# Kernel optimization log

Hardware: AMD Instinct MI355X
Metric: run time of the kernel (lower is better)

## Reference

```python
import jax, jax.numpy as jnp
import numpy as np

S, B, T = 400, 32, 32          # encoder seq len, batch, max_summary_length
V, OOV, E, H = 50000, 50, 128, 256


def _p(key, shape, scale=0.05):
    return (jax.random.normal(key, shape) * scale).astype(jnp.float32)


def lstm_step(x, h, c, Wih, Whh, bih, bhh):
    # PyTorch LSTM gate order: i, f, g, o
    g = x @ Wih.T + h @ Whh.T + bih + bhh
    i, f, gg, o = jnp.split(g, 4, axis=-1)
    c = jax.nn.sigmoid(f) * c + jax.nn.sigmoid(i) * jnp.tanh(gg)
    h = jax.nn.sigmoid(o) * jnp.tanh(c)
    return h, c


def setup_inputs() -> dict:
    key = jax.random.key(0)
    ks = jax.random.split(key, 34)
    inp = {
        # token ids >= 1 so encoder_mask = clip(inputs,0,1) is all ones and
        # packed lengths == full length (PackedRNN becomes a plain LSTM)
        "inputs": jax.random.randint(ks[0], (S, B), 1, V),
        "inputs_lengths": jnp.full((B,), S, dtype=jnp.int32),
        "outputs_tokens": jax.random.randint(ks[1], (T, B), 1, V),  # teacher-forced targets
        "texts_extended": jax.random.randint(ks[2], (S, B), 1, V + OOV),
        "oov_size": OOV,
        # learned parameters
        "embedding": _p(ks[3], (V, E)).at[0].set(0.0),  # padding_idx=0
        "enc_Wih_f": _p(ks[4], (4 * H, E)), "enc_Whh_f": _p(ks[5], (4 * H, H)),
        "enc_bih_f": _p(ks[6], (4 * H,)), "enc_bhh_f": _p(ks[7], (4 * H,)),
        "enc_Wih_b": _p(ks[8], (4 * H, E)), "enc_Whh_b": _p(ks[9], (4 * H, H)),
        "enc_bih_b": _p(ks[10], (4 * H,)), "enc_bhh_b": _p(ks[11], (4 * H,)),
        "W_feat": _p(ks[12], (2 * H, 2 * H)),  # encoder.features (no bias)
        "W_rh": _p(ks[13], (H, 2 * H)), "b_rh": _p(ks[14], (H,)),
        "W_rc": _p(ks[15], (H, 2 * H)), "b_rc": _p(ks[16], (H,)),
        "W_af": _p(ks[17], (2 * H, 2 * H)), "b_af": _p(ks[18], (2 * H,)),  # attention.features
        "w_v": _p(ks[19], (2 * H,)),  # attention_first Linear(2H,1,no bias)
        "W_ctx": _p(ks[20], (E, 2 * H + E)), "b_ctx": _p(ks[21], (E,)),  # decoder.context
        "dec_Wih": _p(ks[22], (4 * H, E)), "dec_Whh": _p(ks[23], (4 * H, H)),
        "dec_bih": _p(ks[24], (4 * H,)), "dec_bhh": _p(ks[25], (4 * H,)),
        "W_pg": _p(ks[26], (1, 4 * H + E)), "b_pg": _p(ks[27], (1,)),
        "W_o1": _p(ks[28], (H, 4 * H)), "b_o1": _p(ks[29], (H,)),
        "W_o2": _p(ks[30], (V, H)), "b_o2": _p(ks[31], (V,)),
    }
    return inp


def reference(inputs, inputs_lengths, outputs_tokens, texts_extended, oov_size,
              embedding, enc_Wih_f, enc_Whh_f, enc_bih_f, enc_bhh_f,
              enc_Wih_b, enc_Whh_b, enc_bih_b, enc_bhh_b,
              W_feat, W_rh, b_rh, W_rc, b_rc, W_af, b_af, w_v,
              W_ctx, b_ctx, dec_Wih, dec_Whh, dec_bih, dec_bhh,
              W_pg, b_pg, W_o1, b_o1, W_o2, b_o2):
    Bsz = inputs.shape[1]
    emb_in = embedding[inputs]                                # [S,B,E]
    h0 = jnp.zeros((Bsz, H), jnp.float32)

    # --- bidirectional encoder LSTM (lengths == S, so packing is a no-op) ---
    def enc_f(carry, x):
        h, c = carry
        h, c = lstm_step(x, h, c, enc_Wih_f, enc_Whh_f, enc_bih_f, enc_bhh_f)
        return (h, c), h

    def enc_b(carry, x):
        h, c = carry
        h, c = lstm_step(x, h, c, enc_Wih_b, enc_Whh_b, enc_bih_b, enc_bhh_b)
        return (h, c), h

    (hf, cf), out_f = jax.lax.scan(enc_f, (h0, h0), emb_in)
    (hb, cb), out_b = jax.lax.scan(enc_b, (h0, h0), emb_in[::-1])
    out_b = out_b[::-1]
    enc_out = jnp.concatenate([out_f, out_b], -1)             # [S,B,2H]
    enc_feat = enc_out @ W_feat.T                             # [S,B,2H]
    dh0 = jax.nn.relu(jnp.concatenate([hf, hb], -1) @ W_rh.T + b_rh)  # [B,H]
    dc0 = jax.nn.relu(jnp.concatenate([cf, cb], -1) @ W_rc.T + b_rc)  # [B,H]

    mask = jnp.clip(inputs, 0, 1).astype(jnp.float32)          # [S,B]
    ctx0 = jnp.zeros((Bsz, 2 * H), jnp.float32)
    rows = jnp.arange(Bsz)[:, None]
    tex_T = texts_extended.T                                   # [B,S]

    # --- decoder loop (teacher forcing, coverage disabled: default) ---
    def dec_step(carry, tok):
        h, c, ctx = carry
        x = jnp.concatenate([ctx, embedding[tok]], 1) @ W_ctx.T + b_ctx     # [B,E]
        h, c = lstm_step(x, h, c, dec_Wih, dec_Whh, dec_bih, dec_bhh)
        dh = jnp.concatenate([h, c], 1)                                      # [B,2H]
        e = jnp.tanh(enc_feat + (dh @ W_af.T + b_af)[None]) @ w_v            # [S,B]
        a = jax.nn.softmax(e, axis=0) * mask
        a = a / a.sum(0, keepdims=True)                                      # layers.Normalize(0)
        context = jnp.einsum('sb,sbd->bd', a, enc_out)                       # [B,2H]
        p_gen = jax.nn.sigmoid(jnp.concatenate([context, dh, x], 1) @ W_pg.T + b_pg)  # [B,1]
        hid = jnp.concatenate([dh, context], 1) @ W_o1.T + b_o1              # [B,H]
        out_v = jax.nn.softmax(hid @ W_o2.T + b_o2, axis=1)                  # [B,V]
        vd = jnp.pad(p_gen * out_v, ((0, 0), (0, oov_size)))                 # [B,V+OOV]
        final = vd.at[rows, tex_T].add((1.0 - p_gen) * a.T)                  # scatter_add copy dist
        return (h, c, context), (final, a)

    _, (outs, atts) = jax.lax.scan(dec_step, (dh0, dc0, ctx0), outputs_tokens)
    return outs, atts  # [T,B,V+OOV], [T,S,B]
```

## Files before the change

kernel.cpp:

```cpp
#include <hip/hip_runtime.h>

#define DEV static __device__ __forceinline__

typedef short  s16x8 __attribute__((ext_vector_type(8)));
typedef float  f32x4 __attribute__((ext_vector_type(4)));
typedef _Float16 h2f __attribute__((ext_vector_type(2)));

constexpr int S = 400, B = 32, T = 32, V = 50000, OOV = 50, E = 128, H = 256;
constexpr int VO = V + OOV, SB = S * B;
constexpr int VP = 50048;

DEV ushort f2bf(float x) {
    union { float f; unsigned u; } a; a.f = x;
    unsigned r = (a.u + 0x7fffu + ((a.u >> 16) & 1u)) >> 16;
    return (ushort)r;
}
DEV float bf2f(unsigned b) {
    union { unsigned u; float f; } a; a.u = b << 16; return a.f;
}
DEV float sigmoidf_(float x) { return 1.0f / (1.0f + __expf(-x)); }
DEV float tanhf_(float x) { float e = __expf(2.0f * x); return 1.0f - 2.0f / (e + 1.0f); }
DEV h2f asH2(unsigned u) { union { unsigned u; h2f h; } x; x.u = u; return x.h; }

#if __has_builtin(__builtin_amdgcn_fdot2)
DEV float dot2(h2f a, h2f b, float c) { return __builtin_amdgcn_fdot2(a, b, c, false); }
#else
DEV float dot2(h2f a, h2f b, float c) { return c + (float)a.x * (float)b.x + (float)a.y * (float)b.y; }
#endif

DEV unsigned f2e4(float v) {
    union { float f; unsigned u; } a; a.f = v;
    unsigned u = a.u + 0x0007FFFFu + ((a.u >> 20) & 1u);
    int e = (int)((u >> 23) & 255) - 127 + 7;
    unsigned m = (u >> 20) & 7u;
    if (e <= 0) return 0u;
    if (e > 15) { e = 15; m = 6; }
    return (unsigned)((e << 3) | m);
}
DEV float e42f(unsigned b) {
    int e = (int)((b >> 3) & 15), m = (int)(b & 7);
    if (e == 0) return (float)m * 1.953125e-3f;
    union { unsigned u; float f; } a;
    a.u = ((unsigned)(e + 120) << 23) | ((unsigned)m << 20);
    return a.f;
}

constexpr size_t SZ_EMB2D  = (size_t)SB * E * 2;
constexpr size_t SZ_WIHCAT = (size_t)2048 * 128 * 2;
constexpr size_t SZ_BIASX  = 2048 * 4;
constexpr size_t SZ_WFEAT  = (size_t)512 * 512 * 2;
constexpr size_t SZ_WO2    = (size_t)V * H * 2;
constexpr size_t SZ_WHH2   = (size_t)2 * 64 * 512 * 16;
constexpr size_t SZ_WCAT   = (size_t)1024 * 896 * 4;
constexpr size_t SZ_BC     = 1024 * 4;
constexpr size_t SZ_CPG    = 256;
constexpr size_t SZ_WRHT   = (size_t)512 * 256 * 4;
constexpr size_t SZ_WRCT   = (size_t)512 * 256 * 4;
constexpr size_t SZ_EMBDEC = (size_t)T * B * E * 4;
constexpr size_t SZ_WZ     = 1664 * 4 + 256;
constexpr size_t SZ_WAFBF  = (size_t)512 * 512 * 2;
constexpr size_t SZ_WO1BF  = (size_t)256 * 1024 * 2;
constexpr size_t SZ_CTXACC = (size_t)(T + 2) * 16384 * 4;
constexpr size_t SZ_SSUM   = (size_t)(T + 2) * 32 * 4 + 256;
constexpr size_t SZ_XALL   = (size_t)T * B * 1024 * 2;
constexpr size_t SZ_EXPS   = (size_t)T * SB * 4;
constexpr size_t SZ_XPROJ  = (size_t)SB * 2048 * 2;
constexpr size_t SZ_ENCOUT = (size_t)SB * 512 * 2;
constexpr size_t SZ_ENCFEAT= (size_t)SB * 512 * 2;
constexpr size_t SZ_HFIN   = (size_t)2 * B * H * 4;
constexpr size_t SZ_HPP    = (size_t)2 * B * H * 4;
constexpr size_t SZ_PGEN   = (size_t)T * B * 4;
constexpr size_t SZ_HIDALL = (size_t)T * B * 256 * 2;

constexpr size_t OFF_EMB2D  = 0;
constexpr size_t OFF_WIHCAT = OFF_EMB2D  + SZ_EMB2D;
constexpr size_t OFF_BIASX  = OFF_WIHCAT + SZ_WIHCAT;
constexpr size_t OFF_WFEAT  = OFF_BIASX  + SZ_BIASX;
constexpr size_t OFF_WO2    = OFF_WFEAT  + SZ_WFEAT;
constexpr size_t OFF_WHH2   = OFF_WO2    + SZ_WO2;
constexpr size_t OFF_WCAT   = OFF_WHH2   + SZ_WHH2;
constexpr size_t OFF_BC     = OFF_WCAT   + SZ_WCAT;
constexpr size_t OFF_CPG    = OFF_BC     + SZ_BC;
constexpr size_t OFF_WRHT   = OFF_CPG    + SZ_CPG;
constexpr size_t OFF_WRCT   = OFF_WRHT   + SZ_WRHT;
constexpr size_t OFF_EMBDEC = OFF_WRCT   + SZ_WRCT;
constexpr size_t OFF_WZ     = OFF_EMBDEC + SZ_EMBDEC;
constexpr size_t OFF_WAFBF  = OFF_WZ     + SZ_WZ;
constexpr size_t OFF_WO1BF  = OFF_WAFBF  + SZ_WAFBF;
constexpr size_t OFF_CTXACC = OFF_WO1BF  + SZ_WO1BF;
constexpr size_t OFF_SSUM   = OFF_CTXACC + SZ_CTXACC;
constexpr size_t OFF_XALL   = OFF_SSUM   + SZ_SSUM;
constexpr size_t OFF_EXPS   = OFF_XALL   + SZ_XALL;
constexpr size_t OFF_XPROJ  = OFF_EXPS   + SZ_EXPS;
constexpr size_t OFF_ENCOUT = OFF_XPROJ  + SZ_XPROJ;
constexpr size_t OFF_ENCFEAT= OFF_ENCOUT + SZ_ENCOUT;
constexpr size_t OFF_HFIN   = OFF_ENCFEAT+ SZ_ENCFEAT;
constexpr size_t OFF_CFIN   = OFF_HFIN   + SZ_HFIN;
constexpr size_t OFF_HPP    = OFF_CFIN   + SZ_HFIN;
constexpr size_t OFF_CPP    = OFF_HPP    + SZ_HPP;
constexpr size_t OFF_PGEN   = OFF_CPP    + SZ_HPP;
constexpr size_t OFF_HIDALL = OFF_PGEN   + SZ_PGEN;
constexpr size_t OFF_PBUF   = OFF_XPROJ;

constexpr long P1 = 2048L*128;
constexpr long P2 = 2048;
constexpr long P3 = 512L*512;
constexpr long P4 = (long)V*H;
constexpr long P5 = 2L*64*512*4;
constexpr long P6 = 1024L*896;
constexpr long P7 = 1;
constexpr long P8 = 1024;
constexpr long P9 = (long)SB*E;
constexpr long P10 = 512L*256;
constexpr long P11 = 512L*256;
constexpr long P12 = 32L*32*128;
constexpr long P13 = 1664;
constexpr long P14 = 512L*512;
constexpr long P15 = 256L*1024;
constexpr long P16 = (long)(T+2)*16384;
constexpr long P17 = (long)(T+2)*32;
constexpr long PREP_TOTAL = P1+P2+P3+P4+P5+P6+P7+P8+P9+P10+P11+P12+P13+P14+P15+P16+P17;

__global__ __launch_bounds__(256)
void prep_kernel(const float* __restrict__ Wih_f, const float* __restrict__ Wih_b,
                 const float* __restrict__ bih_f, const float* __restrict__ bhh_f,
                 const float* __restrict__ bih_b, const float* __restrict__ bhh_b,
                 const float* __restrict__ W_feat, const float* __restrict__ W_o2,
                 const float* __restrict__ Whh_f, const float* __restrict__ Whh_b,
                 const float* __restrict__ dWih, const float* __restrict__ W_ctx,
                 const float* __restrict__ W_pg, const float* __restrict__ b_pg,
                 const float* __restrict__ b_ctx, const float* __restrict__ dbih,
                 const float* __restrict__ dbhh, const float* __restrict__ emb,
                 const int* __restrict__ inputs, const float* __restrict__ dWhh,
                 const float* __restrict__ W_rh, const float* __restrict__ W_rc,
                 const int* __restrict__ toks, const float* __restrict__ W_af,
                 const float* __restrict__ W_o1,
                 ushort* __restrict__ emb2d, ushort* __restrict__ wihcat,
                 float* __restrict__ biasx, ushort* __restrict__ wfeatbf,
                 ushort* __restrict__ wo2bf, unsigned* __restrict__ whh2,
                 float* __restrict__ wcat, float* __restrict__ cpgp,
                 float* __restrict__ bcv, float* __restrict__ wrhT,
                 float* __restrict__ wrcT, float* __restrict__ embdec,
                 float* __restrict__ wz, ushort* __restrict__ wafbf,
                 ushort* __restrict__ wo1bf, float* __restrict__ ctxAcc,
                 float* __restrict__ ssumAll)
{
    long id = (long)blockIdx.x * 256 + threadIdx.x;
    if (id < P1) { int r = id >> 7, e = id & 127;
        float v = (r < 1024) ? Wih_f[r*128+e] : Wih_b[(r-1024)*128+e];
        wihcat[id] = f2bf(v); return; }
    id -= P1;
    if (id < P2) { biasx[id] = (id < 1024) ? bih_f[id]+bhh_f[id] : bih_b[id-1024]+bhh_b[id-1024]; return; }
    id -= P2;
    if (id < P3) { wfeatbf[id] = f2bf(W_feat[id]); return; }
    id -= P3;
    if (id < P4) { wo2bf[id] = f2bf(W_o2[id]); return; }
    id -= P4;
    if (id < P5) {
        int q = id & 3; long r = id >> 2;
        int t = (int)(r & 511); r >>= 9; int c = (int)(r & 63); int dir = (int)(r >> 6);
        int gate = c >> 4, p = c & 15, kh = t & 1;
        int j = t >> 1;
        int k0 = kh * 128 + p * 8 + 2 * q;
        int row = gate * 256 + j;
        const float* W = dir ? Whh_b : Whh_f;
        h2f hv; hv.x = (_Float16)W[(size_t)row*256 + k0]; hv.y = (_Float16)W[(size_t)row*256 + k0 + 1];
        whh2[id] = __builtin_bit_cast(unsigned, hv); return; }
    id -= P5;
    if (id < P6) { int col = (int)(id / 896), k = (int)(id % 896);
        if (k < 640) {
            float acc = 0.f;
            for (int e = 0; e < 128; ++e) acc += dWih[col*128+e] * W_ctx[e*640+k];
            wcat[id] = acc;
        } else wcat[id] = dWhh[(size_t)col*256 + (k - 640)];
        return; }
    id -= P6;
    if (id < P7) { float acc = b_pg[0];
        for (int e = 0; e < 128; ++e) acc += W_pg[1024+e] * b_ctx[e];
        cpgp[0] = acc; return; }
    id -= P7;
    if (id < P8) { float acc = dbih[id] + dbhh[id];
        for (int e = 0; e < 128; ++e) acc += dWih[id*128+e] * b_ctx[e];
        bcv[id] = acc; return; }
    id -= P8;
    if (id < P9) { long sb = id >> 7; int e = id & 127;
        emb2d[id] = f2bf(emb[(size_t)inputs[sb]*128 + e]); return; }
    id -= P9;
    if (id < P10) { int j = id & 255; long k = id >> 8;
        wrhT[id] = W_rh[(size_t)j * 512 + k]; return; }
    id -= P10;
    if (id < P11) { int j = id & 255; long k = id >> 8;
        wrcT[id] = W_rc[(size_t)j * 512 + k]; return; }
    id -= P11;
    if (id < P12) { long tb = id >> 7; int e = id & 127;
        embdec[id] = emb[(size_t)toks[tb]*128 + e]; return; }
    id -= P12;
    if (id < P13) {
        int k = (int)id;
        if (k < 1024) wz[k] = W_pg[k];
        else { int u = k - 1024; float acc = 0.f;
            for (int e = 0; e < 128; ++e) acc += W_pg[1024+e] * W_ctx[e*640+u];
            wz[k] = acc; }
        return; }
    id -= P13;
    if (id < P14) { int d = id & 511; long k = id >> 9;
        wafbf[id] = f2bf(W_af[(size_t)d * 512 + k]); return; }
    id -= P14;
    if (id < P15) { wo1bf[id] = f2bf(W_o1[id]); return; }
    id -= P15;
    if (id < P16) { ctxAcc[id] = 0.f; return; }
    id -= P16;
    if (id < P17) { ssumAll[id] = (id < 64) ? 1.0f : 0.f; return; }
}

template<int BM, int BN, int NT, int MODE, bool BIAS, bool SWZ>
__global__ __launch_bounds__(NT)
void gemm_nt(const ushort* __restrict__ A, int lda, const ushort* __restrict__ Bm, int ldb,
             void* __restrict__ Cp, int ldc, const float* __restrict__ bias,
             int M, int N, int K)
{
    constexpr int WN = BN / 32;
    __shared__ ushort sA[BM * 32];
    __shared__ ushort sB[BN * 32];
    int tid = threadIdx.x, lane = tid & 63, wid = tid >> 6;
    int wm = wid / WN, wn = wid % WN;
    int mb = blockIdx.y, nb = blockIdx.x;
    if (SWZ) {
        int n = gridDim.x, x = nb & 7, y = nb >> 3, q = n >> 3, r = n & 7;
        nb = (x < r ? x * (q + 1) : r * (q + 1) + (x - r) * q) + y;
    }
    int l15 = lane & 15, lg = lane >> 4;
    f32x4 acc[2][2] = {};
    for (int k0 = 0; k0 < K; k0 += 32) {
        for (int idx = tid; idx < BM * 4; idx += NT) {
            int r = idx >> 2, kc = (idx & 3) << 3;
            int row = mb * BM + r;
            uint4 v = make_uint4(0u, 0u, 0u, 0u);
            if (row < M) v = *(const uint4*)(A + (size_t)row * lda + k0 + kc);
            *(uint4*)(&sA[r * 32 + kc]) = v;
        }
        for (int idx = tid; idx < BN * 4; idx += NT) {
            int r = idx >> 2, kc = (idx & 3) << 3;
            int row = nb * BN + r;
            uint4 v = make_uint4(0u, 0u, 0u, 0u);
            if (row < N) v = *(const uint4*)(Bm + (size_t)row * ldb + k0 + kc);
            *(uint4*)(&sB[r * 32 + kc]) = v;
        }
        __syncthreads();
        s16x8 a0 = *(const s16x8*)(&sA[(wm * 32 + l15) * 32 + lg * 8]);
        s16x8 a1 = *(const s16x8*)(&sA[(wm * 32 + 16 + l15) * 32 + lg * 8]);
        s16x8 b0 = *(const s16x8*)(&sB[(wn * 32 + l15) * 32 + lg * 8]);
        s16x8 b1 = *(const s16x8*)(&sB[(wn * 32 + 16 + l15) * 32 + lg * 8]);
        acc[0][0] = __builtin_amdgcn_mfma_f32_16x16x32_bf16(a0, b0, acc[0][0], 0, 0, 0);
        acc[0][1] = __builtin_amdgcn_mfma_f32_16x16x32_bf16(a0, b1, acc[0][1], 0, 0, 0);
        acc[1][0] = __builtin_amdgcn_mfma_f32_16x16x32_bf16(a1, b0, acc[1][0], 0, 0, 0);
        acc[1][1] = __builtin_amdgcn_mfma_f32_16x16x32_bf16(a1, b1, acc[1][1], 0, 0, 0);
        __syncthreads();
    }
    int cb = nb * BN + wn * 32, rb = mb * BM + wm * 32;
    #pragma unroll
    for (int mf = 0; mf < 2; ++mf)
    #pragma unroll
    for (int nf = 0; nf < 2; ++nf) {
        int col = cb + nf * 16 + l15;
        float bv = 0.f;
        if (BIAS) { if (col < N) bv = bias[col]; }
        #pragma unroll
        for (int r = 0; r < 4; ++r) {
            int row = rb + mf * 16 + lg * 4 + r;
            if (row < M && col < N) {
                float v = acc[mf][nf][r] + bv;
                if (MODE == 0)      ((float*)Cp)[(size_t)row * ldc + col] = v;
                else if (MODE == 1) ((ushort*)Cp)[(size_t)row * ldc + col] = __builtin_bit_cast(ushort, (_Float16)v);
                else if (MODE == 2) ((float*)Cp)[(size_t)row * ldc + col] = __expf(v);
                else if (MODE == 3) ((ushort*)Cp)[(size_t)row * ldc + col] = f2bf(v);
                else                ((unsigned char*)Cp)[(size_t)row * ldc + col] = (unsigned char)f2e4(__expf(v));
            }
        }
    }
}

__global__ __launch_bounds__(512, 2)
void enc_kernel(const ushort* __restrict__ xproj, const uint4* __restrict__ whh2,
                ushort* __restrict__ encoutB, float* __restrict__ hfin, float* __restrict__ cfin)
{
    __shared__ uint4  wlds[18 * 512];
    __shared__ __attribute__((aligned(16))) ushort hh16[2][2][136];
    int b = blockIdx.x & 31, dir = blockIdx.x >> 5;
    int t = threadIdx.x, j = t >> 1, kh = t & 1;
    const uint4* gw = whh2 + (size_t)dir * 64 * 512 + t;
    uint4 wreg[46];
    #pragma unroll
    for (int c = 0; c < 46; ++c) wreg[c] = gw[(size_t)c * 512];
    #pragma unroll
    for (int c = 46; c < 64; ++c) wlds[(c - 46) * 512 + t] = gw[(size_t)c * 512];
    if (t < 256) { hh16[0][t >> 7][t & 127] = 0; }
    float cst = 0.f, hst = 0.f;
    __syncthreads();
    const int khoff = kh * 512;
    #pragma unroll 1
    for (int step = 0; step < S; ++step) {
        int s = dir ? (S - 1 - step) : step;
        int cur = step & 1, nxt = cur ^ 1;
        const ushort* xp = xproj + ((size_t)(s * B + b)) * 2048 + dir * 1024 + j + khoff;
        ushort xra = xp[0], xrb = xp[256];
        float a0 = 0.f, a1 = 0.f, a2 = 0.f, a3 = 0.f;
        #pragma unroll
        for (int p = 0; p < 16; ++p) {
            uint4 hp = *(const uint4*)(&hh16[cur][kh][p * 8]);
            uint4 wi = wreg[p];
            uint4 wf = wreg[16 + p];
            uint4 wg = (p < 14) ? wreg[32 + p] : wlds[(p - 14) * 512 + t];
            uint4 wo = wlds[(p + 2) * 512 + t];
            h2f p0 = asH2(hp.x), p1 = asH2(hp.y), p2 = asH2(hp.z), p3 = asH2(hp.w);
            a0 = dot2(p0, asH2(wi.x), a0); a0 = dot2(p1, asH2(wi.y), a0);
            a0 = dot2(p2, asH2(wi.z), a0); a0 = dot2(p3, asH2(wi.w), a0);
            a1 = dot2(p0, asH2(wf.x), a1); a1 = dot2(p1, asH2(wf.y), a1);
            a1 = dot2(p2, asH2(wf.z), a1); a1 = dot2(p3, asH2(wf.w), a1);
            a2 = dot2(p0, asH2(wg.x), a2); a2 = dot2(p1, asH2(wg.y), a2);
            a2 = dot2(p2, asH2(wg.z), a2); a2 = dot2(p3, asH2(wg.w), a2);
            a3 = dot2(p0, asH2(wo.x), a3); a3 = dot2(p1, asH2(wo.y), a3);
            a3 = dot2(p2, asH2(wo.z), a3); a3 = dot2(p3, asH2(wo.w), a3);
        }
        float xv0 = (float)__builtin_bit_cast(_Float16, xra);
        float xv1 = (float)__builtin_bit_cast(_Float16, xrb);
        a0 += kh ? 0.f : xv0;  a1 += kh ? 0.f : xv1;
        a2 += kh ? xv0 : 0.f;  a3 += kh ? xv1 : 0.f;
        a0 += __shfl_xor(a0, 1); a1 += __shfl_xor(a1, 1);
        a2 += __shfl_xor(a2, 1); a3 += __shfl_xor(a3, 1);
        cst = sigmoidf_(a1) * cst + sigmoidf_(a0) * tanhf_(a2);
        hst = sigmoidf_(a3) * tanhf_(cst);
        if (kh == 0) {
            encoutB[((size_t)(b * S + s)) * 512 + dir * 256 + j] = f2bf(hst);
            hh16[nxt][j >> 7][j & 127] = __builtin_bit_cast(ushort, (_Float16)hst);
        }
        __syncthreads();
    }
    if (kh == 0) {
        hfin[(dir * 32 + b) * 256 + j] = hst;
        cfin[(dir * 32 + b) * 256 + j] = cst;
    }
}

__global__ __launch_bounds__(256)
void initdec_kernel(const float* __restrict__ hfin, const float* __restrict__ cfin,
                    const float* __restrict__ wrhT, const float* __restrict__ b_rh,
                    const float* __restrict__ wrcT, const float* __restrict__ b_rc,
                    float* __restrict__ hPP, float* __restrict__ cPP)
{
    int b = blockIdx.x, j = threadIdx.x;
    float ah = b_rh[j], ac = b_rc[j];
    for (int k = 0; k < 512; ++k) {
        float hv = (k < 256) ? hfin[b * 256 + k] : hfin[(32 + b) * 256 + k - 256];
        float cv = (k < 256) ? cfin[b * 256 + k] : cfin[(32 + b) * 256 + k - 256];
        ah += hv * wrhT[k * 256 + j];
        ac += cv * wrcT[k * 256 + j];
    }
    hPP[b * 256 + j] = fmaxf(ah, 0.f);
    cPP[b * 256 + j] = fmaxf(ac, 0.f);
}

__global__ __launch_bounds__(256)
void dec_lstm2_kernel(const float* __restrict__ wcat, const float* __restrict__ bcv,
                      const float* __restrict__ ctxPrevAcc, const float* __restrict__ ssumPrev,
                      const float* __restrict__ hin, const float* __restrict__ cin,
                      float* __restrict__ hout, float* __restrict__ cout,
                      const float* __restrict__ embt, ushort* __restrict__ xAll_t)
{
    __shared__ float pre[256];
    int blk = blockIdx.x, tid = threadIdx.x;
    int b = tid & 31, ci = tid >> 5;
    int gi = ci >> 1, jj = ci & 1;
    int j = (blk << 1) + jj;
    int col = gi * 256 + j;
    float rinvb = 1.0f / ssumPrev[b];
    float acc = bcv[col], accC = 0.f;
    const float4* w = (const float4*)(wcat + (size_t)col * 896);
    const float4* x0 = (const float4*)(ctxPrevAcc + b * 512);
    #pragma unroll 8
    for (int u = 0; u < 128; ++u) { float4 a = w[u], q = x0[u]; accC += a.x*q.x + a.y*q.y + a.z*q.z + a.w*q.w; }
    const float4* x1 = (const float4*)(embt + b * 128);
    #pragma unroll 8
    for (int u = 0; u < 32; ++u) { float4 a = w[128 + u], q = x1[u]; acc += a.x*q.x + a.y*q.y + a.z*q.z + a.w*q.w; }
    const float4* x2 = (const float4*)(hin + b * 256);
    #pragma unroll 8
    for (int u = 0; u < 64; ++u) { float4 a = w[160 + u], q = x2[u]; acc += a.x*q.x + a.y*q.y + a.z*q.z + a.w*q.w; }
    pre[tid] = acc + rinvb * accC;
    __syncthreads();
    if (tid < 64) {
        int b2 = tid & 31, qq = tid >> 5;
        int j2 = (blk << 1) + qq;
        float iv = pre[(0 + qq) * 32 + b2];
        float fv = pre[(2 + qq) * 32 + b2];
        float gv = pre[(4 + qq) * 32 + b2];
        float ov = pre[(6 + qq) * 32 + b2];
        float cp = cin[b2 * 256 + j2];
        float cn = sigmoidf_(fv) * cp + sigmoidf_(iv) * tanhf_(gv);
        float hn = sigmoidf_(ov) * tanhf_(cn);
        cout[b2 * 256 + j2] = cn;
        hout[b2 * 256 + j2] = hn;
        xAll_t[(size_t)b2 * 1024 + j2] = f2bf(hn);
        xAll_t[(size_t)b2 * 1024 + 256 + j2] = f2bf(cn);
    }
}

__global__ __launch_bounds__(512)
void dec_attn2_kernel(const float* __restrict__ h, const float* __restrict__ c,
                      const ushort* __restrict__ wafbf, const float* __restrict__ b_af,
                      const ushort* __restrict__ encfeatB, const float* __restrict__ wv,
                      const int* __restrict__ inputs, const ushort* __restrict__ encoutB,
                      float* __restrict__ expsT, float* __restrict__ ssumT,
                      float* __restrict__ ctxAccT)
{
    __shared__ float hc[512];
    __shared__ float dafL[512];
    __shared__ float scL[50];
    __shared__ float part8[8][512];
    int blk = blockIdx.x, tid = threadIdx.x;
    int b = blk >> 3, sc = blk & 7, s0 = sc * 50;
    int sl = tid >> 6, dth = tid & 63;
    hc[tid] = (tid < 256) ? h[b * 256 + tid] : c[b * 256 + tid - 256];
    __syncthreads();
    {
        float acc8[8] = {};
        const ushort* wbase = wafbf + (size_t)(sl * 64) * 512 + dth * 8;
        #pragma unroll 8
        for (int kk = 0; kk < 64; ++kk) {
            uint4 u = *(const uint4*)(wbase + (size_t)kk * 512);
            float hk = hc[sl * 64 + kk];
            acc8[0] += hk * bf2f(u.x & 0xffffu);
            acc8[1] += hk * bf2f(u.x >> 16);
            acc8[2] += hk * bf2f(u.y & 0xffffu);
            acc8[3] += hk * bf2f(u.y >> 16);
            acc8[4] += hk * bf2f(u.z & 0xffffu);
            acc8[5] += hk * bf2f(u.z >> 16);
            acc8[6] += hk * bf2f(u.w & 0xffffu);
            acc8[7] += hk * bf2f(u.w >> 16);
        }
        #pragma unroll
        for (int jj = 0; jj < 8; ++jj) part8[sl][dth * 8 + jj] = acc8[jj];
    }
    __syncthreads();
    {
        float v = b_af[tid];
        #pragma unroll
        for (int w8 = 0; w8 < 8; ++w8) v += part8[w8][tid];
        dafL[tid] = v;
    }
    __syncthreads();
    float dreg[8], wreg[8];
    #pragma unroll
    for (int jj = 0; jj < 8; ++jj) { dreg[jj] = dafL[dth * 8 + jj]; wreg[jj] = wv[dth * 8 + jj]; }
    for (int i = sl; i < 50; i += 8) {
        int s = s0 + i;
        uint4 u = *(const uint4*)(encfeatB + ((size_t)b * S + s) * 512 + dth * 8);
        h2f e0 = asH2(u.x), e1 = asH2(u.y), e2 = asH2(u.z), e3 = asH2(u.w);
        float e = tanhf_((float)e0.x + dreg[0]) * wreg[0] + tanhf_((float)e0.y + dreg[1]) * wreg[1]
                + tanhf_((float)e1.x + dreg[2]) * wreg[2] + tanhf_((float)e1.y + dreg[3]) * wreg[3]
                + tanhf_((float)e2.x + dreg[4]) * wreg[4] + tanhf_((float)e2.y + dreg[5]) * wreg[5]
                + tanhf_((float)e3.x + dreg[6]) * wreg[6] + tanhf_((float)e3.y + dreg[7]) * wreg[7];
        e += __shfl_xor(e, 1);  e += __shfl_xor(e, 2);
        e += __shfl_xor(e, 4);  e += __shfl_xor(e, 8);
        e += __shfl_xor(e, 16); e += __shfl_xor(e, 32);
        if (dth == 0) {
            float m = (inputs[s * 32 + b] != 0) ? 1.f : 0.f;
            float val = m * __expf(e);
            scL[i] = val;
            expsT[s * 32 + b] = val;
        }
    }
    __syncthreads();
    if (tid == 0) {
        float ss = 0.f;
        for (int i = 0; i < 50; ++i) ss += scL[i];
        atomicAdd(&ssumT[b], ss);
    }
    {
        float acc8[8] = {};
        for (int i = sl; i < 50; i += 8) {
            float a = scL[i];
            uint4 u = *(const uint4*)(encoutB + ((size_t)b * S + s0 + i) * 512 + dth * 8);
            acc8[0] += a * bf2f(u.x & 0xffffu);
            acc8[1] += a * bf2f(u.x >> 16);
            acc8[2] += a * bf2f(u.y & 0xffffu);
            acc8[3] += a * bf2f(u.y >> 16);
            acc8[4] += a * bf2f(u.z & 0xffffu);
            acc8[5] += a * bf2f(u.z >> 16);
            acc8[6] += a * bf2f(u.w & 0xffffu);
            acc8[7] += a * bf2f(u.w >> 16);
        }
        #pragma unroll
        for (int jj = 0; jj < 8; ++jj) part8[sl][dth * 8 + jj] = acc8[jj];
    }
    __syncthreads();
    {
        float v = 0.f;
        #pragma unroll
        for (int s8 = 0; s8 < 8; ++s8) v += part8[s8][tid];
        atomicAdd(&ctxAccT[b * 512 + tid], v);
    }
}

__global__ __launch_bounds__(256)
void cvt_kernel(const float* __restrict__ ctxAcc, const float* __restrict__ ssumAll,
                ushort* __restrict__ xAll)
{
    int id = blockIdx.x * 256 + threadIdx.x;
    int t = id >> 14, rem = id & 16383;
    int b = rem >> 9, k = rem & 511;
    float v = ctxAcc[(size_t)(2 + t) * 16384 + rem] / ssumAll[(2 + t) * 32 + b];
    xAll[(size_t)(t * 32 + b) * 1024 + 512 + k] = f2bf(v);
}

__global__ __launch_bounds__(256)
void pgen_kernel(const ushort* __restrict__ xAll, const float* __restrict__ ctxAcc,
                 const float* __restrict__ ssumAll, const float* __restrict__ embdec,
                 const float* __restrict__ wz, const float* __restrict__ cpgp,
                 float* __restrict__ pgenAll)
{
    int row = blockIdx.x * 8 + (threadIdx.x >> 5);
    int sub = threadIdx.x & 31;
    int t = row >> 5, b = row & 31;
    float rT = 1.0f / ssumAll[(2 + t) * 32 + b];
    float rP = 1.0f / ssumAll[(1 + t) * 32 + b];
    const float* cT = ctxAcc + (size_t)(2 + t) * 16384 + b * 512;
    const float* cP = ctxAcc + (size_t)(1 + t) * 16384 + b * 512;
    const ushort* hx = xAll + (size_t)row * 1024;
    const float* em = embdec + (size_t)row * 128;
    float acc = 0.f;
    for (int k = sub; k < 1664; k += 32) {
        float zv;
        if (k < 512)        zv = cT[k] * rT;
        else if (k < 1024)  zv = bf2f(hx[k - 512]);
        else if (k < 1536)  zv = cP[k - 1024] * rP;
        else                zv = em[k - 1536];
        acc += wz[k] * zv;
    }
    acc += __shfl_xor(acc, 1); acc += __shfl_xor(acc, 2);
    acc += __shfl_xor(acc, 4); acc += __shfl_xor(acc, 8);
    acc += __shfl_xor(acc, 16);
    if (sub == 0) pgenAll[row] = sigmoidf_(acc + cpgp[0]);
}

__global__ __launch_bounds__(256)
void dec_out3_kernel(const unsigned char* __restrict__ pbuf, const float* __restrict__ pgenAll,
                     const int* __restrict__ tex, const float* __restrict__ expsAll,
                     const float* __restrict__ ssumAll,
                     float* __restrict__ outsAll, float* __restrict__ attsAll)
{
    int tb = blockIdx.x, t = threadIdx.x;
    int tstep = tb >> 5, b = tb & 31;
    const unsigned char* prow = pbuf + (size_t)tb * VP;
    float part = 0.f;
    for (int i = t; i < V / 8; i += 256) {
        uint2 u = *(const uint2*)(prow + i * 8);
        unsigned w0 = u.x, w1 = u.y;
        part += e42f(w0 & 255) + e42f((w0 >> 8) & 255) + e42f((w0 >> 16) & 255) + e42f(w0 >> 24);
        part += e42f(w1 & 255) + e42f((w1 >> 8) & 255) + e42f((w1 >> 16) & 255) + e42f(w1 >> 24);
    }
    __shared__ float red[256];
    red[t] = part;
    __syncthreads();
    for (int o = 128; o > 0; o >>= 1) { if (t < o) red[t] += red[t + o]; __syncthreads(); }
    float pg = pgenAll[tb];
    float sca = pg / red[0];
    float om = 1.f - pg;
    float rinv = 1.0f / ssumAll[(2 + tstep) * 32 + b];
    float* orow = outsAll + (size_t)tstep * B * VO + (size_t)b * VO;
    for (int i = t; i < V / 8; i += 256) {
        uint2 u = *(const uint2*)(prow + i * 8);
        unsigned w0 = u.x, w1 = u.y;
        float2* o2 = (float2*)(orow + i * 8);
        o2[0] = make_float2(e42f(w0 & 255) * sca, e42f((w0 >> 8) & 255) * sca);
        o2[1] = make_float2(e42f((w0 >> 16) & 255) * sca, e42f(w0 >> 24) * sca);
        o2[2] = make_float2(e42f(w1 & 255) * sca, e42f((w1 >> 8) & 255) * sca);
        o2[3] = make_float2(e42f((w1 >> 16) & 255) * sca, e42f(w1 >> 24) * sca);
    }
    if (t < OOV) orow[V + t] = 0.f;
    __syncthreads();
    const float* expst = expsAll + (size_t)tstep * SB;
    float* attst = attsAll + (size_t)tstep * SB;
    for (int si = t; si < 400; si += 256) {
        float an = expst[si * 32 + b] * rinv;
        attst[si * 32 + b] = an;
        atomicAdd(orow + tex[si * 32 + b], om * an);
    }
}

extern "C" void kernel_launch(void* const* d_in, const int* in_sizes, int n_in,
                              void* d_out, int out_size, void* d_ws, size_t ws_size,
                              hipStream_t stream)
{
    const int*   inputs  = (const int*)d_in[0];
    const int*   toksAll = (const int*)d_in[2];
    const int*   tex     = (const int*)d_in[3];
    const float* emb     = (const float*)d_in[5];
    const float* Wih_f   = (const float*)d_in[6];
    const float* Whh_f   = (const float*)d_in[7];
    const float* bih_f   = (const float*)d_in[8];
    const float* bhh_f   = (const float*)d_in[9];
    const float* Wih_b   = (const float*)d_in[10];
    const float* Whh_b   = (const float*)d_in[11];
    const float* bih_b   = (const float*)d_in[12];
    const float* bhh_b   = (const float*)d_in[13];
    const float* W_feat  = (const float*)d_in[14];
    const float* W_rh    = (const float*)d_in[15];
    const float* b_rh    = (const float*)d_in[16];
    const float* W_rc    = (const float*)d_in[17];
    const float* b_rc    = (const float*)d_in[18];
    const float* W_af    = (const float*)d_in[19];
    const float* b_af    = (const float*)d_in[20];
    const float* w_v     = (const float*)d_in[21];
    const float* W_ctx   = (const float*)d_in[22];
    const float* b_ctx   = (const float*)d_in[23];
    const float* dWih    = (const float*)d_in[24];
    const float* dWhh    = (const float*)d_in[25];
    const float* dbih    = (const float*)d_in[26];
    const float* dbhh    = (const float*)d_in[27];
    const float* W_pg    = (const float*)d_in[28];
    const float* b_pg    = (const float*)d_in[29];
    const float* W_o1    = (const float*)d_in[30];
    const float* b_o1    = (const float*)d_in[31];
    const float* W_o2    = (const float*)d_in[32];
    const float* b_o2    = (const float*)d_in[33];

    char* wsb = (char*)d_ws;
    ushort*   emb2d   = (ushort*)(wsb + OFF_EMB2D);
    ushort*   wihcat  = (ushort*)(wsb + OFF_WIHCAT);
    float*    biasx   = (float*)(wsb + OFF_BIASX);
    ushort*   wfeatbf = (ushort*)(wsb + OFF_WFEAT);
    ushort*   wo2bf   = (ushort*)(wsb + OFF_WO2);
    unsigned* whh2    = (unsigned*)(wsb + OFF_WHH2);
    float*    wcat    = (float*)(wsb + OFF_WCAT);
    float*    bcv     = (float*)(wsb + OFF_BC);
    float*    cpgp    = (float*)(wsb + OFF_CPG);
    float*    wrhT    = (float*)(wsb + OFF_WRHT);
    float*    wrcT    = (float*)(wsb + OFF_WRCT);
    float*    embdec  = (float*)(wsb + OFF_EMBDEC);
    float*    wz      = (float*)(wsb + OFF_WZ);
    ushort*   wafbf   = (ushort*)(wsb + OFF_WAFBF);
    ushort*   wo1bf   = (ushort*)(wsb + OFF_WO1BF);
    float*    ctxAcc  = (float*)(wsb + OFF_CTXACC);
    float*    ssumAll = (float*)(wsb + OFF_SSUM);
    ushort*   xAll    = (ushort*)(wsb + OFF_XALL);
    float*    expsAll = (float*)(wsb + OFF_EXPS);
    ushort*   xproj   = (ushort*)(wsb + OFF_XPROJ);
    ushort*   encoutB = (ushort*)(wsb + OFF_ENCOUT);
    ushort*   encfeatB= (ushort*)(wsb + OFF_ENCFEAT);
    float*    hfin    = (float*)(wsb + OFF_HFIN);
    float*    cfin    = (float*)(wsb + OFF_CFIN);
    float*    hPP     = (float*)(wsb + OFF_HPP);
    float*    cPP     = (float*)(wsb + OFF_CPP);
    float*    pgenAll = (float*)(wsb + OFF_PGEN);
    ushort*   hidAll  = (ushort*)(wsb + OFF_HIDALL);
    unsigned char* pbuf = (unsigned char*)(wsb + OFF_PBUF);

    float* outs = (float*)d_out;
    float* atts = outs + (size_t)T * B * VO;

    int prep_blocks = (int)((PREP_TOTAL + 255) / 256);
    prep_kernel<<<prep_blocks, 256, 0, stream>>>(
        Wih_f, Wih_b, bih_f, bhh_f, bih_b, bhh_b, W_feat, W_o2, Whh_f, Whh_b,
        dWih, W_ctx, W_pg, b_pg, b_ctx, dbih, dbhh, emb, inputs, dWhh, W_rh, W_rc,
        toksAll, W_af, W_o1,
        emb2d, wihcat, biasx, wfeatbf, wo2bf, whh2, wcat, cpgp, bcv, wrhT, wrcT,
        embdec, wz, wafbf, wo1bf, ctxAcc, ssumAll);

    gemm_nt<64, 64, 256, 1, true, false><<<dim3(2048 / 64, SB / 64), 256, 0, stream>>>(
        emb2d, 128, wihcat, 128, (void*)xproj, 2048, biasx, SB, 2048, 128);

    enc_kernel<<<64, 512, 0, stream>>>(xproj, (const uint4*)whh2, encoutB, hfin, cfin);

    initdec_kernel<<<32, 256, 0, stream>>>(hfin, cfin, wrhT, b_rh, wrcT, b_rc, hPP, cPP);

    gemm_nt<64, 64, 256, 1, false, false><<<dim3(512 / 64, SB / 64), 256, 0, stream>>>(
        encoutB, 512, wfeatbf, 512, (void*)encfeatB, 512, nullptr, SB, 512, 512);

    for (int t = 0; t < T; ++t) {
        int p = t & 1, q = p ^ 1;
        float* hin = hPP + (size_t)p * 8192;
        float* cin = cPP + (size_t)p * 8192;
        float* hout = hPP + (size_t)q * 8192;
        float* cout = cPP + (size_t)q * 8192;
        dec_lstm2_kernel<<<128, 256, 0, stream>>>(
            wcat, bcv,
            ctxAcc + (size_t)(t + 1) * 16384, ssumAll + (t + 1) * 32,
            hin, cin, hout, cout,
            embdec + (size_t)t * 4096, xAll + (size_t)t * 32768);
        dec_attn2_kernel<<<256, 512, 0, stream>>>(
            hout, cout, wafbf, b_af, encfeatB, w_v, inputs, encoutB,
            expsAll + (size_t)t * SB, ssumAll + (2 + t) * 32,
            ctxAcc + (size_t)(2 + t) * 16384);
    }
    cvt_kernel<<<(T * B * 512) / 256, 256, 0, stream>>>(ctxAcc, ssumAll, xAll);
    pgen_kernel<<<128, 256, 0, stream>>>(xAll, ctxAcc, ssumAll, embdec, wz, cpgp, pgenAll);
    gemm_nt<64, 64, 256, 3, true, false><<<dim3(256 / 64, 1024 / 64), 256, 0, stream>>>(
        xAll, 1024, wo1bf, 1024, (void*)hidAll, 256, b_o1, T * B, 256, 1024);
    gemm_nt<64, 128, 512, 4, true, true><<<dim3(391, 16), 512, 0, stream>>>(
        hidAll, 256, wo2bf, 256, (void*)pbuf, VP, b_o2, T * B, V, 256);
    dec_out3_kernel<<<T * B, 256, 0, stream>>>(pbuf, pgenAll, tex, expsAll, ssumAll, outs, atts);
}
```

Before: 2.876 ms.

## Fuse decoder LSTM and attention steps using a precomputed encoder-context projection

Merges the per-step decoder LSTM kernel and the attention kernel into a single kernel, halving the kernel launches inside the time loop. To avoid needing the previous step's finished context vector, it precomputes a per-position projection of the encoder outputs (enc_out times the combined W_ctx and decoder input weights) as an fp16 GEMM. Each step then forms the context contribution to the gates as an exp-weighted sum over source positions, which is the same algebra reordered. The fused kernel runs only 64 blocks, and both blocks of a batch row redo the LSTM gate work. Each block also streams a large fp16 tensor every step, so memory traffic and serialization rise in exchange for fewer launches.

```diff
diff --git a/kernel.cpp b/kernel.cpp
--- a/kernel.cpp
+++ b/kernel.cpp
@@ -18,6 +18,7 @@
 DEV float bf2f(unsigned b) {
     union { unsigned u; float f; } a; a.u = b << 16; return a.f;
 }
+DEV float f16f(unsigned u16) { return (float)__builtin_bit_cast(_Float16, (ushort)u16); }
 DEV float sigmoidf_(float x) { return 1.0f / (1.0f + __expf(-x)); }
 DEV float tanhf_(float x) { float e = __expf(2.0f * x); return 1.0f - 2.0f / (e + 1.0f); }
 DEV h2f asH2(unsigned u) { union { unsigned u; h2f h; } x; x.u = u; return x.h; }
@@ -51,7 +52,8 @@
 constexpr size_t SZ_WFEAT  = (size_t)512 * 512 * 2;
 constexpr size_t SZ_WO2    = (size_t)V * H * 2;
 constexpr size_t SZ_WHH2   = (size_t)2 * 64 * 512 * 16;
-constexpr size_t SZ_WCAT   = (size_t)1024 * 896 * 4;
+constexpr size_t SZ_WLSTMT = (size_t)384 * 1024 * 4;
+constexpr size_t SZ_WCTXBF = (size_t)1024 * 512 * 2;
 constexpr size_t SZ_BC     = 1024 * 4;
 constexpr size_t SZ_CPG    = 256;
 constexpr size_t SZ_WRHT   = (size_t)512 * 256 * 4;
@@ -63,7 +65,7 @@
 constexpr size_t SZ_CTXACC = (size_t)(T + 2) * 16384 * 4;
 constexpr size_t SZ_SSUM   = (size_t)(T + 2) * 32 * 4 + 256;
 constexpr size_t SZ_XALL   = (size_t)T * B * 1024 * 2;
-constexpr size_t SZ_EXPS   = (size_t)T * SB * 4;
+constexpr size_t SZ_EXPS   = (size_t)(T + 1) * SB * 4;
 constexpr size_t SZ_XPROJ  = (size_t)SB * 2048 * 2;
 constexpr size_t SZ_ENCOUT = (size_t)SB * 512 * 2;
 constexpr size_t SZ_ENCFEAT= (size_t)SB * 512 * 2;
@@ -78,8 +80,9 @@
 constexpr size_t OFF_WFEAT  = OFF_BIASX  + SZ_BIASX;
 constexpr size_t OFF_WO2    = OFF_WFEAT  + SZ_WFEAT;
 constexpr size_t OFF_WHH2   = OFF_WO2    + SZ_WO2;
-constexpr size_t OFF_WCAT   = OFF_WHH2   + SZ_WHH2;
-constexpr size_t OFF_BC     = OFF_WCAT   + SZ_WCAT;
+constexpr size_t OFF_WLSTMT = OFF_WHH2   + SZ_WHH2;
+constexpr size_t OFF_WCTXBF = OFF_WLSTMT + SZ_WLSTMT;
+constexpr size_t OFF_BC     = OFF_WCTXBF + SZ_WCTXBF;
 constexpr size_t OFF_CPG    = OFF_BC     + SZ_BC;
 constexpr size_t OFF_WRHT   = OFF_CPG    + SZ_CPG;
 constexpr size_t OFF_WRCT   = OFF_WRHT   + SZ_WRHT;
@@ -100,6 +103,7 @@
 constexpr size_t OFF_CPP    = OFF_HPP    + SZ_HPP;
 constexpr size_t OFF_PGEN   = OFF_CPP    + SZ_HPP;
 constexpr size_t OFF_HIDALL = OFF_PGEN   + SZ_PGEN;
+constexpr size_t OFF_ENCW   = OFF_XPROJ;
 constexpr size_t OFF_PBUF   = OFF_XPROJ;
 
 constexpr long P1 = 2048L*128;
@@ -107,7 +111,7 @@
 constexpr long P3 = 512L*512;
 constexpr long P4 = (long)V*H;
 constexpr long P5 = 2L*64*512*4;
-constexpr long P6 = 1024L*896;
+constexpr long P6 = 384L*1024;
 constexpr long P7 = 1;
 constexpr long P8 = 1024;
 constexpr long P9 = (long)SB*E;
@@ -119,7 +123,9 @@
 constexpr long P15 = 256L*1024;
 constexpr long P16 = (long)(T+2)*16384;
 constexpr long P17 = (long)(T+2)*32;
-constexpr long PREP_TOTAL = P1+P2+P3+P4+P5+P6+P7+P8+P9+P10+P11+P12+P13+P14+P15+P16+P17;
+constexpr long P18 = 1024L*512;
+constexpr long P19 = (long)SB;
+constexpr long PREP_TOTAL = P1+P2+P3+P4+P5+P6+P7+P8+P9+P10+P11+P12+P13+P14+P15+P16+P17+P18+P19;
 
 __global__ __launch_bounds__(256)
 void prep_kernel(const float* __restrict__ Wih_f, const float* __restrict__ Wih_b,
@@ -138,12 +144,13 @@
                  ushort* __restrict__ emb2d, ushort* __restrict__ wihcat,
                  float* __restrict__ biasx, ushort* __restrict__ wfeatbf,
                  ushort* __restrict__ wo2bf, unsigned* __restrict__ whh2,
-                 float* __restrict__ wcat, float* __restrict__ cpgp,
+                 float* __restrict__ wlstmT, float* __restrict__ cpgp,
                  float* __restrict__ bcv, float* __restrict__ wrhT,
                  float* __restrict__ wrcT, float* __restrict__ embdec,
                  float* __restrict__ wz, ushort* __restrict__ wafbf,
                  ushort* __restrict__ wo1bf, float* __restrict__ ctxAcc,
-                 float* __restrict__ ssumAll)
+                 float* __restrict__ ssumAll, ushort* __restrict__ wcatCtxBf,
+                 float* __restrict__ expsAll)
 {
     long id = (long)blockIdx.x * 256 + threadIdx.x;
     if (id < P1) { int r = id >> 7, e = id & 127;
@@ -167,13 +174,13 @@
         h2f hv; hv.x = (_Float16)W[(size_t)row*256 + k0]; hv.y = (_Float16)W[(size_t)row*256 + k0 + 1];
         whh2[id] = __builtin_bit_cast(unsigned, hv); return; }
     id -= P5;
-    if (id < P6) { int col = (int)(id / 896), k = (int)(id % 896);
-        if (k < 640) {
-            float acc = 0.f;
-            for (int e = 0; e < 128; ++e) acc += dWih[col*128+e] * W_ctx[e*640+k];
-            wcat[id] = acc;
-        } else wcat[id] = dWhh[(size_t)col*256 + (k - 640)];
-        return; }
+    if (id < P6) { int k = (int)(id >> 10), col = (int)(id & 1023);
+        float v;
+        if (k < 128) { float acc = 0.f;
+            for (int e = 0; e < 128; ++e) acc += dWih[col*128+e] * W_ctx[e*640+512+k];
+            v = acc;
+        } else v = dWhh[(size_t)col*256 + (k - 128)];
+        wlstmT[id] = v; return; }
     id -= P6;
     if (id < P7) { float acc = b_pg[0];
         for (int e = 0; e < 128; ++e) acc += W_pg[1024+e] * b_ctx[e];
@@ -211,6 +218,13 @@
     if (id < P16) { ctxAcc[id] = 0.f; return; }
     id -= P16;
     if (id < P17) { ssumAll[id] = (id < 64) ? 1.0f : 0.f; return; }
+    id -= P17;
+    if (id < P18) { int col = (int)(id >> 9), k = (int)(id & 511);
+        float acc = 0.f;
+        for (int e = 0; e < 128; ++e) acc += dWih[col*128+e] * W_ctx[e*640+k];
+        wcatCtxBf[id] = f2bf(acc); return; }
+    id -= P18;
+    if (id < P19) { expsAll[id] = 0.f; return; }
 }
 
 template<int BM, int BN, int NT, int MODE, bool BIAS, bool SWZ>
@@ -274,6 +288,7 @@
                 else if (MODE == 1) ((ushort*)Cp)[(size_t)row * ldc + col] = __builtin_bit_cast(ushort, (_Float16)v);
                 else if (MODE == 2) ((float*)Cp)[(size_t)row * ldc + col] = __expf(v);
                 else if (MODE == 3) ((ushort*)Cp)[(size_t)row * ldc + col] = f2bf(v);
+                else if (MODE == 5) ((ushort*)Cp)[(size_t)row * ldc + (((col & 511) << 1) | (col >> 9))] = __builtin_bit_cast(ushort, (_Float16)v);
                 else                ((unsigned char*)Cp)[(size_t)row * ldc + col] = (unsigned char)f2e4(__expf(v));
             }
         }
@@ -360,66 +375,68 @@
     cPP[b * 256 + j] = fmaxf(ac, 0.f);
 }
 
-__global__ __launch_bounds__(256)
-void dec_lstm2_kernel(const float* __restrict__ wcat, const float* __restrict__ bcv,
-                      const float* __restrict__ ctxPrevAcc, const float* __restrict__ ssumPrev,
+__global__ __launch_bounds__(512)
+void dec_fused_kernel(const float* __restrict__ wlstmT, const float* __restrict__ bcv,
+                      const ushort* __restrict__ encW2,
+                      const float* __restrict__ expsPrev, const float* __restrict__ ssumPrev,
+                      const float* __restrict__ embt,
                       const float* __restrict__ hin, const float* __restrict__ cin,
                       float* __restrict__ hout, float* __restrict__ cout,
-                      const float* __restrict__ embt, ushort* __restrict__ xAll_t)
-{
-    __shared__ float pre[256];
-    int blk = blockIdx.x, tid = threadIdx.x;
-    int b = tid & 31, ci = tid >> 5;
-    int gi = ci >> 1, jj = ci & 1;
-    int j = (blk << 1) + jj;
-    int col = gi * 256 + j;
-    float rinvb = 1.0f / ssumPrev[b];
-    float acc = bcv[col], accC = 0.f;
-    const float4* w = (const float4*)(wcat + (size_t)col * 896);
-    const float4* x0 = (const float4*)(ctxPrevAcc + b * 512);
-    #pragma unroll 8
-    for (int u = 0; u < 128; ++u) { float4 a = w[u], q = x0[u]; accC += a.x*q.x + a.y*q.y + a.z*q.z + a.w*q.w; }
-    const float4* x1 = (const float4*)(embt + b * 128);
-    #pragma unroll 8
-    for (int u = 0; u < 32; ++u) { float4 a = w[128 + u], q = x1[u]; acc += a.x*q.x + a.y*q.y + a.z*q.z + a.w*q.w; }
-    const float4* x2 = (const float4*)(hin + b * 256);
-    #pragma unroll 8
-    for (int u = 0; u < 64; ++u) { float4 a = w[160 + u], q = x2[u]; acc += a.x*q.x + a.y*q.y + a.z*q.z + a.w*q.w; }
-    pre[tid] = acc + rinvb * accC;
-    __syncthreads();
-    if (tid < 64) {
-        int b2 = tid & 31, qq = tid >> 5;
-        int j2 = (blk << 1) + qq;
-        float iv = pre[(0 + qq) * 32 + b2];
-        float fv = pre[(2 + qq) * 32 + b2];
-        float gv = pre[(4 + qq) * 32 + b2];
-        float ov = pre[(6 + qq) * 32 + b2];
-        float cp = cin[b2 * 256 + j2];
-        float cn = sigmoidf_(fv) * cp + sigmoidf_(iv) * tanhf_(gv);
-        float hn = sigmoidf_(ov) * tanhf_(cn);
-        cout[b2 * 256 + j2] = cn;
-        hout[b2 * 256 + j2] = hn;
-        xAll_t[(size_t)b2 * 1024 + j2] = f2bf(hn);
-        xAll_t[(size_t)b2 * 1024 + 256 + j2] = f2bf(cn);
-    }
-}
-
-__global__ __launch_bounds__(512)
-void dec_attn2_kernel(const float* __restrict__ h, const float* __restrict__ c,
+                      ushort* __restrict__ xAll_t,
                       const ushort* __restrict__ wafbf, const float* __restrict__ b_af,
                       const ushort* __restrict__ encfeatB, const float* __restrict__ wv,
                       const int* __restrict__ inputs, const ushort* __restrict__ encoutB,
                       float* __restrict__ expsT, float* __restrict__ ssumT,
                       float* __restrict__ ctxAccT)
 {
+    __shared__ float xv[384];
+    __shared__ float epv[400];
+    __shared__ float gl[1024];
     __shared__ float hc[512];
     __shared__ float dafL[512];
-    __shared__ float scL[50];
+    __shared__ float scL[200];
     __shared__ float part8[8][512];
+    __shared__ float redn[512];
     int blk = blockIdx.x, tid = threadIdx.x;
-    int b = blk >> 3, sc = blk & 7, s0 = sc * 50;
+    int b = blk >> 1, half = blk & 1, s0 = half * 200;
     int sl = tid >> 6, dth = tid & 63;
-    hc[tid] = (tid < 256) ? h[b * 256 + tid] : c[b * 256 + tid - 256];
+    if (tid < 128) xv[tid] = embt[b * 128 + tid];
+    else if (tid < 384) xv[tid] = hin[b * 256 + (tid - 128)];
+    if (tid < 400) epv[tid] = expsPrev[tid * 32 + b];
+    __syncthreads();
+    {
+        float rinv = 1.0f / ssumPrev[b];
+        float a0 = bcv[tid], a1 = bcv[tid + 512];
+        #pragma unroll 4
+        for (int k = 0; k < 384; ++k) {
+            float x = xv[k];
+            a0 += x * wlstmT[k * 1024 + tid];
+            a1 += x * wlstmT[k * 1024 + 512 + tid];
+        }
+        float e0 = 0.f, e1 = 0.f;
+        const ushort* er = encW2 + (size_t)b * S * 1024 + tid * 2;
+        #pragma unroll 4
+        for (int s = 0; s < 400; ++s) {
+            unsigned u = *(const unsigned*)(er + (size_t)s * 1024);
+            float w = epv[s];
+            e0 += w * f16f(u & 0xffffu);
+            e1 += w * f16f(u >> 16);
+        }
+        gl[tid] = a0 + rinv * e0;
+        gl[tid + 512] = a1 + rinv * e1;
+    }
+    __syncthreads();
+    if (tid < 256) {
+        float gi = gl[tid], gf = gl[256 + tid], gg = gl[512 + tid], go = gl[768 + tid];
+        float cp = cin[b * 256 + tid];
+        float cn = sigmoidf_(gf) * cp + sigmoidf_(gi) * tanhf_(gg);
+        float hn = sigmoidf_(go) * tanhf_(cn);
+        cout[b * 256 + tid] = cn;
+        hout[b * 256 + tid] = hn;
+        hc[tid] = hn; hc[256 + tid] = cn;
+        xAll_t[(size_t)b * 1024 + tid] = f2bf(hn);
+        xAll_t[(size_t)b * 1024 + 256 + tid] = f2bf(cn);
+    }
     __syncthreads();
     {
         float acc8[8] = {};
@@ -451,7 +468,7 @@
     float dreg[8], wreg[8];
     #pragma unroll
     for (int jj = 0; jj < 8; ++jj) { dreg[jj] = dafL[dth * 8 + jj]; wreg[jj] = wv[dth * 8 + jj]; }
-    for (int i = sl; i < 50; i += 8) {
+    for (int i = sl; i < 200; i += 8) {
         int s = s0 + i;
         uint4 u = *(const uint4*)(encfeatB + ((size_t)b * S + s) * 512 + dth * 8);
         h2f e0 = asH2(u.x), e1 = asH2(u.y), e2 = asH2(u.z), e3 = asH2(u.w);
@@ -470,14 +487,13 @@
         }
     }
     __syncthreads();
-    if (tid == 0) {
-        float ss = 0.f;
-        for (int i = 0; i < 50; ++i) ss += scL[i];
-        atomicAdd(&ssumT[b], ss);
-    }
+    redn[tid] = (tid < 200) ? scL[tid] : 0.f;
+    __syncthreads();
+    for (int o = 256; o > 0; o >>= 1) { if (tid < o) redn[tid] += redn[tid + o]; __syncthreads(); }
+    if (tid == 0) atomicAdd(ssumT + b, redn[0]);
     {
         float acc8[8] = {};
-        for (int i = sl; i < 50; i += 8) {
+        for (int i = sl; i < 200; i += 8) {
             float a = scL[i];
             uint4 u = *(const uint4*)(encoutB + ((size_t)b * S + s0 + i) * 512 + dth * 8);
             acc8[0] += a * bf2f(u.x & 0xffffu);
@@ -497,7 +513,7 @@
         float v = 0.f;
         #pragma unroll
         for (int s8 = 0; s8 < 8; ++s8) v += part8[s8][tid];
-        atomicAdd(&ctxAccT[b * 512 + tid], v);
+        atomicAdd(ctxAccT + (size_t)b * 512 + tid, v);
     }
 }
 
@@ -578,7 +594,7 @@
     }
     if (t < OOV) orow[V + t] = 0.f;
     __syncthreads();
-    const float* expst = expsAll + (size_t)tstep * SB;
+    const float* expst = expsAll + (size_t)(1 + tstep) * SB;
     float* attst = attsAll + (size_t)tstep * SB;
     for (int si = t; si < 400; si += 256) {
         float an = expst[si * 32 + b] * rinv;
@@ -631,7 +647,8 @@
     ushort*   wfeatbf = (ushort*)(wsb + OFF_WFEAT);
     ushort*   wo2bf   = (ushort*)(wsb + OFF_WO2);
     unsigned* whh2    = (unsigned*)(wsb + OFF_WHH2);
-    float*    wcat    = (float*)(wsb + OFF_WCAT);
+    float*    wlstmT  = (float*)(wsb + OFF_WLSTMT);
+    ushort*   wcatCtxBf = (ushort*)(wsb + OFF_WCTXBF);
     float*    bcv     = (float*)(wsb + OFF_BC);
     float*    cpgp    = (float*)(wsb + OFF_CPG);
     float*    wrhT    = (float*)(wsb + OFF_WRHT);
@@ -645,6 +662,7 @@
     ushort*   xAll    = (ushort*)(wsb + OFF_XALL);
     float*    expsAll = (float*)(wsb + OFF_EXPS);
     ushort*   xproj   = (ushort*)(wsb + OFF_XPROJ);
+    ushort*   encW2   = (ushort*)(wsb + OFF_ENCW);
     ushort*   encoutB = (ushort*)(wsb + OFF_ENCOUT);
     ushort*   encfeatB= (ushort*)(wsb + OFF_ENCFEAT);
     float*    hfin    = (float*)(wsb + OFF_HFIN);
@@ -663,8 +681,8 @@
         Wih_f, Wih_b, bih_f, bhh_f, bih_b, bhh_b, W_feat, W_o2, Whh_f, Whh_b,
         dWih, W_ctx, W_pg, b_pg, b_ctx, dbih, dbhh, emb, inputs, dWhh, W_rh, W_rc,
         toksAll, W_af, W_o1,
-        emb2d, wihcat, biasx, wfeatbf, wo2bf, whh2, wcat, cpgp, bcv, wrhT, wrcT,
-        embdec, wz, wafbf, wo1bf, ctxAcc, ssumAll);
+        emb2d, wihcat, biasx, wfeatbf, wo2bf, whh2, wlstmT, cpgp, bcv, wrhT, wrcT,
+        embdec, wz, wafbf, wo1bf, ctxAcc, ssumAll, wcatCtxBf, expsAll);
 
     gemm_nt<64, 64, 256, 1, true, false><<<dim3(2048 / 64, SB / 64), 256, 0, stream>>>(
         emb2d, 128, wihcat, 128, (void*)xproj, 2048, biasx, SB, 2048, 128);
@@ -675,6 +693,9 @@
 
     gemm_nt<64, 64, 256, 1, false, false><<<dim3(512 / 64, SB / 64), 256, 0, stream>>>(
         encoutB, 512, wfeatbf, 512, (void*)encfeatB, 512, nullptr, SB, 512, 512);
+
+    gemm_nt<64, 64, 256, 5, false, false><<<dim3(1024 / 64, SB / 64), 256, 0, stream>>>(
+        encoutB, 512, wcatCtxBf, 512, (void*)encW2, 1024, nullptr, SB, 1024, 512);
 
     for (int t = 0; t < T; ++t) {
         int p = t & 1, q = p ^ 1;
@@ -682,14 +703,13 @@
         float* cin = cPP + (size_t)p * 8192;
         float* hout = hPP + (size_t)q * 8192;
         float* cout = cPP + (size_t)q * 8192;
-        dec_lstm2_kernel<<<128, 256, 0, stream>>>(
-            wcat, bcv,
-            ctxAcc + (size_t)(t + 1) * 16384, ssumAll + (t + 1) * 32,
-            hin, cin, hout, cout,
-            embdec + (size_t)t * 4096, xAll + (size_t)t * 32768);
-        dec_attn2_kernel<<<256, 512, 0, stream>>>(
-            hout, cout, wafbf, b_af, encfeatB, w_v, inputs, encoutB,
-            expsAll + (size_t)t * SB, ssumAll + (2 + t) * 32,
+        dec_fused_kernel<<<64, 512, 0, stream>>>(
+            wlstmT, bcv, encW2,
+            expsAll + (size_t)t * SB, ssumAll + (t + 1) * 32,
+            embdec + (size_t)t * 4096,
+            hin, cin, hout, cout, xAll + (size_t)t * 32768,
+            wafbf, b_af, encfeatB, w_v, inputs, encoutB,
+            expsAll + (size_t)(t + 1) * SB, ssumAll + (t + 2) * 32,
             ctxAcc + (size_t)(2 + t) * 16384);
     }
     cvt_kernel<<<(T * B * 512) / 256, 256, 0, stream>>>(ctxAcc, ssumAll, xAll);
```

New measurement: 4.743 ms. 1.65x slower.
